# Kernel tuning notes

Hardware: AMD Instinct MI355X
Metric: run time of the kernel (lower is better)

The kernel has to match this reference:

```python
import jax, jax.numpy as jnp
import numpy as np

CUTOFF = 5.0
P_ENV = 5.0  # envelope exponent


def _build_triplets(src, dst, num_nodes):
    # Faithful numpy port of DimeNet.triplets (row=src=j, col=dst=i).
    # For each edge e=(j->i), enumerate in-edges f=(k->j) of node j, drop k==i.
    E = src.shape[0]
    order = np.argsort(dst, kind='stable')          # edge ids grouped by target node
    indeg = np.bincount(dst, minlength=num_nodes)
    ptr = np.concatenate([np.zeros(1, np.int64), np.cumsum(indeg)])
    counts = indeg[src]                              # num_triplets per edge e
    total = int(counts.sum())
    idx_ji = np.repeat(np.arange(E), counts)
    grp_start = np.repeat(np.cumsum(counts) - counts, counts)
    pos_in = np.arange(total) - grp_start
    idx_kj = order[ptr[src][idx_ji] + pos_in]        # in-edge ids f of node j
    idx_k = src[idx_kj]
    idx_j = src[idx_ji]
    idx_i = dst[idx_ji]
    mask = idx_i != idx_k
    return idx_i[mask], idx_j[mask], idx_k[mask]


def setup_inputs() -> dict:
    rng = np.random.default_rng(0)
    N, E, IN, H, NR, OUT = 50000, 400000, 128, 128, 6, 64
    src = rng.integers(0, N, E)
    dst = rng.integers(0, N, E)
    dst = np.where(dst == src, (dst + 1) % N, dst)   # no self loops
    idx_i, idx_j, idx_k = _build_triplets(src, dst, N)

    def W(*shape):
        fan_in = shape[-1]
        return jnp.asarray((rng.standard_normal(shape) / np.sqrt(fan_in)).astype(np.float32))

    return {
        'x': jnp.asarray(rng.standard_normal((N, IN)).astype(np.float32)),
        'pos': jnp.asarray((rng.standard_normal((N, 3)) * 3.0).astype(np.float32)),
        'freq': jnp.asarray(np.pi * np.arange(1, NR + 1, dtype=np.float32)),
        'Wx': jnp.asarray(rng.uniform(-np.sqrt(3), np.sqrt(3), (H, IN)).astype(np.float32)),
        'Wr': W(H, NR), 'br': jnp.zeros((H,), jnp.float32),
        'Wl': W(H, 3 * H), 'bl': jnp.zeros((H,), jnp.float32),
        'Wrbf': W(H, NR),
        'Wls': W(3, H, H), 'bls': jnp.zeros((3, H), jnp.float32),
        'Wout': W(OUT, H),
        'edge_src': jnp.asarray(src.astype(np.int32)),
        'edge_dst': jnp.asarray(dst.astype(np.int32)),
        'idx_i': jnp.asarray(idx_i.astype(np.int32)),
        'idx_j': jnp.asarray(idx_j.astype(np.int32)),
        'idx_k': jnp.asarray(idx_k.astype(np.int32)),
    }


def reference(x, pos, freq, Wx, Wr, br, Wl, bl, Wrbf, Wls, bls, Wout,
              edge_src, edge_dst, idx_i, idx_j, idx_k):
    swish = lambda t: t * jax.nn.sigmoid(t)
    num_nodes = x.shape[0]

    # edge distances: j,i = edge_index; dist = |pos[i]-pos[j]|
    d = jnp.sqrt(jnp.sum((pos[edge_dst] - pos[edge_src]) ** 2, axis=-1))  # [E]

    # triplet angles (computed as in original forward; sbf is a no-op)
    pi_ = pos[idx_i]
    v_ji = pos[idx_j] - pi_
    v_ki = pos[idx_k] - pi_
    a = jnp.sum(v_ji * v_ki, axis=-1)
    b = jnp.linalg.norm(jnp.cross(v_ji, v_ki), axis=-1)
    angle = jnp.arctan2(b, a)  # [T]

    # Bessel basis with polynomial envelope
    dn = (d / CUTOFF)[:, None]  # [E,1]
    p = P_ENV
    A = -(p + 1.0) * (p + 2.0) / 2.0
    B = p * (p + 2.0)
    C = -p * (p + 1.0) / 2.0
    dp = dn ** p
    env = 1.0 / dn + A * dp + B * dp * dn + C * dp * dn * dn
    rbf = env * jnp.sin(freq * dn)  # [E, NR]

    # EmbeddingBlock
    h = x @ Wx.T                                  # [N,H]
    rbf_h = swish(rbf @ Wr.T + br)                # [E,H]
    e = swish(jnp.concatenate([h[edge_dst], h[edge_src], rbf_h], axis=-1) @ Wl.T + bl)  # [E,H]

    # OutputBlock 0
    t = (rbf @ Wrbf.T) * e                        # [E,H]
    node = jax.ops.segment_sum(t, edge_dst, num_segments=num_nodes)  # [N,H]
    for k in range(Wls.shape[0]):
        node = swish(node @ Wls[k].T + bls[k])
    P = node @ Wout.T                             # [N,OUT]
    return P, angle
```

## Files before the change

kernel.cpp:

```cpp
#include <hip/hip_runtime.h>
#include <hip/hip_bf16.h>
#include <math.h>

#define H   128
#define NR  6
#define NOUT 64

typedef __attribute__((ext_vector_type(8))) short short8;
typedef __attribute__((ext_vector_type(4))) float floatx4;

__device__ __forceinline__ float swishf(float z) {
  float t = __expf(-z);
  return z * __builtin_amdgcn_rcpf(1.0f + t);
}

__device__ __forceinline__ ushort f2bf(float x) {
  __hip_bfloat16 b = __float2bfloat16(x);
  return *reinterpret_cast<ushort*>(&b);
}

__device__ __forceinline__ ushort f2bf_rne(float x) {
  unsigned int u = __float_as_uint(x);
  u += 0x7FFFu + ((u >> 16) & 1u);
  return (ushort)(u >> 16);
}

__device__ __forceinline__ float bf2f(ushort u) {
  unsigned int v = ((unsigned int)u) << 16;
  return __uint_as_float(v);
}

__device__ __forceinline__ void async_copy16(const void* g, void* l) {
  __builtin_amdgcn_global_load_lds(
      (const __attribute__((address_space(1))) unsigned int*)g,
      (__attribute__((address_space(3))) unsigned int*)l, 16, 0, 0);
}

__global__ void k_init(float4* __restrict__ nodeA, int n4, int* __restrict__ cnt, int n,
                       const float* __restrict__ Wl, const float* __restrict__ Wx,
                       const float* __restrict__ Wls, const float* __restrict__ Wout,
                       ushort* __restrict__ Wlbf,
                       ushort* __restrict__ Wxhi, ushort* __restrict__ Wxlo,
                       ushort* __restrict__ Wlshi, ushort* __restrict__ Wlslo,
                       ushort* __restrict__ Wouthi, ushort* __restrict__ Woutlo) {
  int i = blockIdx.x * blockDim.x + threadIdx.x;
  if (i < n4) nodeA[i] = make_float4(0.f, 0.f, 0.f, 0.f);
  if (i < n) cnt[i] = 0;
  int idx = i;
  if (idx < 49152) {
    Wlbf[idx] = f2bf(Wl[idx]);
    return;
  }
  idx -= 49152;
  if (idx < 16384) {
    float x = Wx[idx];
    ushort h = f2bf(x);
    Wxhi[idx] = h; Wxlo[idx] = f2bf(x - bf2f(h));
    return;
  }
  idx -= 16384;
  if (idx < 49152) {
    float x = Wls[idx];
    ushort h = f2bf(x);
    Wlshi[idx] = h; Wlslo[idx] = f2bf(x - bf2f(h));
    return;
  }
  idx -= 49152;
  if (idx < 8192) {
    float x = Wout[idx];
    ushort h = f2bf(x);
    Wouthi[idx] = h; Woutlo[idx] = f2bf(x - bf2f(h));
  }
}

__global__ void k_hist(const int* __restrict__ dst, int* __restrict__ cnt, int E) {
  int i = blockIdx.x * blockDim.x + threadIdx.x;
  if (i < E) atomicAdd(&cnt[dst[i]], 1);
}

__global__ __launch_bounds__(1024) void k_scanA(const int* __restrict__ cnt,
                                                int* __restrict__ cur,
                                                int* __restrict__ bsum, int N) {
  __shared__ int wsum[16];
  const int tid = threadIdx.x;
  const int gid = blockIdx.x * 1024 + tid;
  const int lane = tid & 63, wv = tid >> 6;
  int v0 = (gid < N) ? cnt[gid] : 0;
  int v = v0;
#pragma unroll
  for (int off = 1; off < 64; off <<= 1) {
    int t = __shfl_up(v, off, 64);
    if (lane >= off) v += t;
  }
  if (lane == 63) wsum[wv] = v;
  __syncthreads();
  if (wv == 0 && lane < 16) {
    int t = wsum[lane];
#pragma unroll
    for (int off = 1; off < 16; off <<= 1) {
      int u2 = __shfl_up(t, off, 64);
      if (lane >= off) t += u2;
    }
    wsum[lane] = t;
  }
  __syncthreads();
  int excl = (wv > 0 ? wsum[wv - 1] : 0) + (v - v0);
  if (gid < N) cur[gid] = excl;
  if (tid == 0) bsum[blockIdx.x] = wsum[15];
}

__global__ __launch_bounds__(256) void k_scatter_feat_ang(
    const float* __restrict__ pos, const int* __restrict__ esrc,
    const int* __restrict__ edst, const float* __restrict__ freq,
    int* __restrict__ cur, const int* __restrict__ bsum, int nscan,
    float* __restrict__ epk,
    int E, int EB,
    const int* __restrict__ ii, const int* __restrict__ jj, const int* __restrict__ kk,
    float* __restrict__ ang, int T) {
  if (blockIdx.x < (unsigned)EB) {
    __shared__ int boffS[64];
    {
      const int lane = threadIdx.x & 63;
      if (threadIdx.x < 64) {
        int v = (lane < nscan) ? bsum[lane] : 0;
        int v0 = v;
#pragma unroll
        for (int off = 1; off < 64; off <<= 1) {
          int t = __shfl_up(v, off, 64);
          if (lane >= off) v += t;
        }
        boffS[lane] = v - v0;
      }
    }
    __syncthreads();
    int i = blockIdx.x * 256 + threadIdx.x;
    if (i >= E) return;
    const int s = esrc[i], d = edst[i];
    const int p = atomicAdd(&cur[d], 1) + boffS[d >> 10];
    float dx = pos[d * 3 + 0] - pos[s * 3 + 0];
    float dy = pos[d * 3 + 1] - pos[s * 3 + 1];
    float dz = pos[d * 3 + 2] - pos[s * 3 + 2];
    float dist = sqrtf(dx * dx + dy * dy + dz * dz);
    float dn = dist * 0.2f;
    float inv = __builtin_amdgcn_rcpf(dn);
    float dn2 = dn * dn;
    float dp = dn2 * dn2 * dn;
    float env = inv - 21.0f * dp + 35.0f * dp * dn - 15.0f * dp * dn2;
    float rb[NR];
#pragma unroll
    for (int r = 0; r < NR; ++r) rb[r] = env * __sinf(freq[r] * dn);
    float4 w0 = make_float4(rb[0], rb[1], rb[2], rb[3]);
    float4 w1 = make_float4(rb[4], rb[5], __int_as_float(s), __int_as_float(d));
    *(float4*)&epk[(size_t)p * 8] = w0;
    *(float4*)&epk[(size_t)p * 8 + 4] = w1;
  } else {
    int t = (blockIdx.x - EB) * 256 + threadIdx.x;
    if (t >= T) return;
    int i = ii[t], j = jj[t], k = kk[t];
    float pix = pos[i * 3], piy = pos[i * 3 + 1], piz = pos[i * 3 + 2];
    float vjx = pos[j * 3] - pix, vjy = pos[j * 3 + 1] - piy, vjz = pos[j * 3 + 2] - piz;
    float vkx = pos[k * 3] - pix, vky = pos[k * 3 + 1] - piy, vkz = pos[k * 3 + 2] - piz;
    float a = vjx * vkx + vjy * vky + vjz * vkz;
    float cx = vjy * vkz - vjz * vky;
    float cy = vjz * vkx - vjx * vkz;
    float cz = vjx * vky - vjy * vkx;
    float b = sqrtf(cx * cx + cy * cy + cz * cz);
    ang[t] = atan2f(b, a);
  }
}

__global__ __launch_bounds__(512, 4) void k_x_gemm(
    const float* __restrict__ A,
    const ushort* __restrict__ Bhi,
    const ushort* __restrict__ Blo,
    ushort* __restrict__ C,
    int M) {
  __shared__ alignas(16) ushort Ah[128 * 32];
  __shared__ alignas(16) ushort Al[128 * 32];
  __shared__ alignas(16) ushort Bh[128 * 32];
  __shared__ alignas(16) ushort Bl[128 * 32];

  const int tid = threadIdx.x;
  const int m0 = blockIdx.x * 128;
  const int w = tid >> 6, lane = tid & 63;
  const int l15 = lane & 15, quad = lane >> 4;
  const int wm = (w >> 1) * 32;
  const int wn = (w & 1) * 64;

  floatx4 acc[2][4];
#pragma unroll
  for (int i = 0; i < 2; ++i)
#pragma unroll
    for (int j = 0; j < 4; ++j) acc[i][j] = floatx4{0.f, 0.f, 0.f, 0.f};

  for (int c = 0; c < 4; ++c) {
    const int kb = c * 32;
    {
      int row = tid >> 2, g = tid & 3;
      int m = m0 + row;
      float4 v0 = make_float4(0.f, 0.f, 0.f, 0.f), v1 = v0;
      if (m < M) {
        v0 = *(const float4*)&A[(size_t)m * 128 + kb + g * 8];
        v1 = *(const float4*)&A[(size_t)m * 128 + kb + g * 8 + 4];
      }
      float xs[8] = {v0.x, v0.y, v0.z, v0.w, v1.x, v1.y, v1.z, v1.w};
      short8 hi, lo;
#pragma unroll
      for (int j = 0; j < 8; ++j) {
        ushort h = f2bf_rne(xs[j]);
        hi[j] = (short)h;
        lo[j] = (short)f2bf_rne(xs[j] - bf2f(h));
      }
      int slot = row * 4 + (g ^ ((row >> 1) & 3));
      *(short8*)(Ah + slot * 8) = hi;
      *(short8*)(Al + slot * 8) = lo;
    }
    {
      int s = w * 64 + lane;
      int brow = s >> 2, gp = s & 3;
      int gg = gp ^ ((brow >> 1) & 3);
      int lb = __builtin_amdgcn_readfirstlane(w * 64);
      async_copy16((const void*)(Bhi + (size_t)brow * 128 + kb + gg * 8), (void*)(Bh + lb * 8));
      async_copy16((const void*)(Blo + (size_t)brow * 128 + kb + gg * 8), (void*)(Bl + lb * 8));
    }
    __syncthreads();
    short8 ah[2], al[2], bh[4], blv[4];
#pragma unroll
    for (int i = 0; i < 2; ++i) {
      int m = wm + i * 16 + l15;
      int slot = m * 4 + (quad ^ ((m >> 1) & 3));
      ah[i] = *(const short8*)(Ah + slot * 8);
      al[i] = *(const short8*)(Al + slot * 8);
    }
#pragma unroll
    for (int j = 0; j < 4; ++j) {
      int n = wn + j * 16 + l15;
      int slot = n * 4 + (quad ^ ((n >> 1) & 3));
      bh[j] = *(const short8*)(Bh + slot * 8);
      blv[j] = *(const short8*)(Bl + slot * 8);
    }
#pragma unroll
    for (int i = 0; i < 2; ++i)
#pragma unroll
      for (int j = 0; j < 4; ++j) {
        acc[i][j] = __builtin_amdgcn_mfma_f32_16x16x32_bf16(ah[i], bh[j], acc[i][j], 0, 0, 0);
        acc[i][j] = __builtin_amdgcn_mfma_f32_16x16x32_bf16(ah[i], blv[j], acc[i][j], 0, 0, 0);
        acc[i][j] = __builtin_amdgcn_mfma_f32_16x16x32_bf16(al[i], bh[j], acc[i][j], 0, 0, 0);
      }
    __syncthreads();
  }

#pragma unroll
  for (int i = 0; i < 2; ++i)
#pragma unroll
    for (int r = 0; r < 4; ++r) {
      int m = m0 + wm + i * 16 + quad * 4 + r;
      if (m < M) {
#pragma unroll
        for (int j = 0; j < 4; ++j) {
          int n = wn + j * 16 + l15;
          C[(size_t)m * 128 + n] = f2bf_rne(acc[i][j][r]);
        }
      }
    }
}

__global__ __launch_bounds__(512, 4) void k_node_mlp(
    const float* __restrict__ nodeA,
    const ushort* __restrict__ Wlshi,
    const ushort* __restrict__ Wlslo,
    const ushort* __restrict__ Wouthi,
    const ushort* __restrict__ Woutlo,
    const float* __restrict__ bls,
    float* __restrict__ P,
    int M) {
  __shared__ alignas(16) ushort AactH[64 * 16 * 8];
  __shared__ alignas(16) ushort AactL[64 * 16 * 8];
  __shared__ alignas(16) ushort Bh[128 * 4 * 8];
  __shared__ alignas(16) ushort Bl[128 * 4 * 8];
  __shared__ float blsS[3 * 128];

  const int tid = threadIdx.x;
  const int m0 = blockIdx.x * 64;
  const int w = tid >> 6, lane = tid & 63;
  const int l15 = lane & 15, quad = lane >> 4;
  const int wm = (w >> 2) * 32;
  const int wn = (w & 3) * 32;

  for (int i = tid; i < 3 * 128; i += 512) blsS[i] = bls[i];

  floatx4 acc[2][2];

  for (int p = 0; p < 3; ++p) {
    const ushort* Bhg = Wlshi + p * 128 * 128;
    const ushort* Blg = Wlslo + p * 128 * 128;
#pragma unroll
    for (int i = 0; i < 2; ++i)
#pragma unroll
      for (int j = 0; j < 2; ++j) acc[i][j] = floatx4{0.f, 0.f, 0.f, 0.f};

    for (int c = 0; c < 4; ++c) {
      const int kb = c * 32;
      {
        int s = w * 64 + lane;
        int brow = s >> 2, gp = s & 3;
        int gg = gp ^ ((brow >> 1) & 3);
        int lb = __builtin_amdgcn_readfirstlane(w * 64);
        async_copy16((const void*)(Bhg + (size_t)brow * 128 + kb + gg * 8), (void*)(Bh + lb * 8));
        async_copy16((const void*)(Blg + (size_t)brow * 128 + kb + gg * 8), (void*)(Bl + lb * 8));
      }
      __syncthreads();
      short8 ah[2], al[2];
      if (p == 0) {
#pragma unroll
        for (int i = 0; i < 2; ++i) {
          int m = m0 + wm + i * 16 + l15;
          float4 v0 = make_float4(0.f, 0.f, 0.f, 0.f), v1 = v0;
          if (m < M) {
            v0 = *(const float4*)&nodeA[(size_t)m * 128 + kb + quad * 8];
            v1 = *(const float4*)&nodeA[(size_t)m * 128 + kb + quad * 8 + 4];
          }
          float xs[8] = {v0.x, v0.y, v0.z, v0.w, v1.x, v1.y, v1.z, v1.w};
#pragma unroll
          for (int j = 0; j < 8; ++j) {
            ushort hh = f2bf_rne(xs[j]);
            ah[i][j] = (short)hh;
            al[i][j] = (short)f2bf_rne(xs[j] - bf2f(hh));
          }
        }
      } else {
#pragma unroll
        for (int i = 0; i < 2; ++i) {
          int arow = wm + i * 16 + l15;
          int g16 = c * 4 + quad;
          int slot = arow * 16 + (g16 ^ (arow & 15));
          ah[i] = *(const short8*)(AactH + slot * 8);
          al[i] = *(const short8*)(AactL + slot * 8);
        }
      }
      short8 bh[2], blv[2];
#pragma unroll
      for (int j = 0; j < 2; ++j) {
        int n = wn + j * 16 + l15;
        int slot = n * 4 + (quad ^ ((n >> 1) & 3));
        bh[j] = *(const short8*)(Bh + slot * 8);
        blv[j] = *(const short8*)(Bl + slot * 8);
      }
#pragma unroll
      for (int i = 0; i < 2; ++i)
#pragma unroll
        for (int j = 0; j < 2; ++j) {
          acc[i][j] = __builtin_amdgcn_mfma_f32_16x16x32_bf16(ah[i], bh[j], acc[i][j], 0, 0, 0);
          acc[i][j] = __builtin_amdgcn_mfma_f32_16x16x32_bf16(ah[i], blv[j], acc[i][j], 0, 0, 0);
          acc[i][j] = __builtin_amdgcn_mfma_f32_16x16x32_bf16(al[i], bh[j], acc[i][j], 0, 0, 0);
        }
      __syncthreads();
    }
#pragma unroll
    for (int i = 0; i < 2; ++i)
#pragma unroll
      for (int r = 0; r < 4; ++r) {
        int row = wm + i * 16 + quad * 4 + r;
#pragma unroll
        for (int j = 0; j < 2; ++j) {
          int col = wn + j * 16 + l15;
          float z = acc[i][j][r] + blsS[p * 128 + col];
          z = swishf(z);
          ushort hh = f2bf_rne(z);
          int slot = row * 16 + ((col >> 3) ^ (row & 15));
          AactH[slot * 8 + (col & 7)] = hh;
          AactL[slot * 8 + (col & 7)] = f2bf_rne(z - bf2f(hh));
        }
      }
    __syncthreads();
  }

  const int wn3 = (w & 3) * 16;
#pragma unroll
  for (int i = 0; i < 2; ++i) acc[i][0] = floatx4{0.f, 0.f, 0.f, 0.f};

  for (int c = 0; c < 4; ++c) {
    const int kb = c * 32;
    if (w < 4) {
      int s = w * 64 + lane;
      int brow = s >> 2, gp = s & 3;
      int gg = gp ^ ((brow >> 1) & 3);
      int lb = __builtin_amdgcn_readfirstlane(w * 64);
      async_copy16((const void*)(Wouthi + (size_t)brow * 128 + kb + gg * 8), (void*)(Bh + lb * 8));
      async_copy16((const void*)(Woutlo + (size_t)brow * 128 + kb + gg * 8), (void*)(Bl + lb * 8));
    }
    __syncthreads();
    short8 ah[2], al[2], bh, blv;
#pragma unroll
    for (int i = 0; i < 2; ++i) {
      int arow = wm + i * 16 + l15;
      int g16 = c * 4 + quad;
      int slot = arow * 16 + (g16 ^ (arow & 15));
      ah[i] = *(const short8*)(AactH + slot * 8);
      al[i] = *(const short8*)(AactL + slot * 8);
    }
    {
      int n = wn3 + l15;
      int slot = n * 4 + (quad ^ ((n >> 1) & 3));
      bh = *(const short8*)(Bh + slot * 8);
      blv = *(const short8*)(Bl + slot * 8);
    }
#pragma unroll
    for (int i = 0; i < 2; ++i) {
      acc[i][0] = __builtin_amdgcn_mfma_f32_16x16x32_bf16(ah[i], bh, acc[i][0], 0, 0, 0);
      acc[i][0] = __builtin_amdgcn_mfma_f32_16x16x32_bf16(ah[i], blv, acc[i][0], 0, 0, 0);
      acc[i][0] = __builtin_amdgcn_mfma_f32_16x16x32_bf16(al[i], bh, acc[i][0], 0, 0, 0);
    }
    __syncthreads();
  }
#pragma unroll
  for (int i = 0; i < 2; ++i)
#pragma unroll
    for (int r = 0; r < 4; ++r) {
      int m = m0 + wm + i * 16 + quad * 4 + r;
      if (m < M) {
        int n = wn3 + l15;
        P[(size_t)m * NOUT + n] = acc[i][0][r];
      }
    }
}

__global__ __launch_bounds__(512, 4) void k_edge_mfma(
    const ushort* __restrict__ hbf,
    const ushort* __restrict__ Wlbf,
    const float* __restrict__ bl,
    const float* __restrict__ epk,
    const float* __restrict__ Wr,
    const float* __restrict__ br,
    const float* __restrict__ Wrbf,
    float* __restrict__ node,
    int E, int nb, int perXcd) {
  __shared__ alignas(16) ushort ABs[33280];
  __shared__ float rbfS[128][6];
  __shared__ int dstS[128];
  __shared__ int srcS[128];

  const int bp = blockIdx.x;
  const int lb = (bp & 7) * perXcd + (bp >> 3);
  if (lb >= nb) return;

  ushort* As = ABs;
  ushort* Bs = ABs + 128 * 16 * 8;

  const int tid = threadIdx.x;
  const int e0 = lb * 128;

  if (tid < 128) {
    int e = min(e0 + tid, E - 1);
    const float* rec = epk + (size_t)e * 8;
    float4 r0 = *(const float4*)rec;
    float4 r1 = *(const float4*)(rec + 4);
    bool ok = (e0 + tid < E);
    rbfS[tid][0] = ok ? r0.x : 0.f;
    rbfS[tid][1] = ok ? r0.y : 0.f;
    rbfS[tid][2] = ok ? r0.z : 0.f;
    rbfS[tid][3] = ok ? r0.w : 0.f;
    rbfS[tid][4] = ok ? r1.x : 0.f;
    rbfS[tid][5] = ok ? r1.y : 0.f;
    srcS[tid] = __float_as_int(r1.z);
    dstS[tid] = __float_as_int(r1.w);
  }
  __syncthreads();

  const int w = tid >> 6;
  const int lane = tid & 63;
  const int l15 = lane & 15, quad = lane >> 4;
  const int wm = (w >> 1) * 32;
  const int wn = (w & 1) * 64;

  floatx4 acc[2][4];
#pragma unroll
  for (int i = 0; i < 2; ++i)
#pragma unroll
    for (int j = 0; j < 4; ++j) acc[i][j] = floatx4{0.f, 0.f, 0.f, 0.f};

  for (int c = 0; c < 3; ++c) {
#pragma unroll
    for (int i = 0; i < 4; ++i) {
      int u = w * 256 + i * 64 + lane;
      int nrow = u >> 4, gp = u & 15;
      int g = gp ^ (nrow & 15);
      const ushort* gsrc = Wlbf + (size_t)nrow * 384 + c * 128 + g * 8;
      int lbo = __builtin_amdgcn_readfirstlane(w * 256 + i * 64);
      async_copy16((const void*)gsrc, (void*)(Bs + lbo * 8));
    }
    if (c < 2) {
      const int* rowS = (c == 0) ? dstS : srcS;
#pragma unroll
      for (int i = 0; i < 4; ++i) {
        int u = w * 256 + i * 64 + lane;
        int nrow = u >> 4;
        int g = (u & 15) ^ (nrow & 15);
        int row = rowS[nrow];
        const ushort* gsrc = hbf + (size_t)row * H + g * 8;
        int lbo = __builtin_amdgcn_readfirstlane(w * 256 + i * 64);
        async_copy16((const void*)gsrc, (void*)(As + lbo * 8));
      }
    } else {
      const int colL = tid & 127;
      float w0 = Wr[colL * NR + 0], w1 = Wr[colL * NR + 1], w2 = Wr[colL * NR + 2];
      float w3 = Wr[colL * NR + 3], w4 = Wr[colL * NR + 4], w5 = Wr[colL * NR + 5];
      float bv = br[colL];
      const int r0 = (tid >> 7) * 32;
#pragma unroll
      for (int r = 0; r < 32; ++r) {
        int m = r0 + r;
        const float2* rp = (const float2*)&rbfS[m][0];
        float2 q0 = rp[0], q1 = rp[1], q2 = rp[2];
        float z = bv + q0.x * w0 + q0.y * w1 + q1.x * w2 + q1.y * w3 + q2.x * w4 + q2.y * w5;
        ushort hv = f2bf_rne(swishf(z));
        As[(m * 16 + ((colL >> 3) ^ (m & 15))) * 8 + (colL & 7)] = hv;
      }
    }
    __syncthreads();
#pragma unroll
    for (int s = 0; s < 4; ++s) {
      const int gg = s * 4 + quad;
      short8 af[2], bfr[4];
#pragma unroll
      for (int i = 0; i < 2; ++i) {
        int m = wm + i * 16 + l15;
        af[i] = *(const short8*)(As + (m * 16 + (gg ^ (m & 15))) * 8);
      }
#pragma unroll
      for (int j = 0; j < 4; ++j) {
        int n = wn + j * 16 + l15;
        bfr[j] = *(const short8*)(Bs + (n * 16 + (gg ^ (n & 15))) * 8);
      }
#pragma unroll
      for (int i = 0; i < 2; ++i)
#pragma unroll
        for (int j = 0; j < 4; ++j)
          acc[i][j] = __builtin_amdgcn_mfma_f32_16x16x32_bf16(af[i], bfr[j], acc[i][j], 0, 0, 0);
    }
    __syncthreads();
  }

  float* redS = (float*)ABs;
  float wt[4][NR], blv[4];
#pragma unroll
  for (int j = 0; j < 4; ++j) {
    int n = wn + j * 16 + l15;
    blv[j] = bl[n];
#pragma unroll
    for (int r = 0; r < NR; ++r) wt[j][r] = Wrbf[n * NR + r];
  }

#pragma unroll
  for (int i = 0; i < 2; ++i)
#pragma unroll
    for (int r = 0; r < 4; ++r) {
      int mg = wm + i * 16 + quad * 4 + r;
      float rb[NR];
#pragma unroll
      for (int q = 0; q < NR; ++q) rb[q] = rbfS[mg][q];
#pragma unroll
      for (int j = 0; j < 4; ++j) {
        float z = acc[i][j][r] + blv[j];
        float ev = swishf(z);
        float wv = 0.f;
#pragma unroll
        for (int q = 0; q < NR; ++q) wv += rb[q] * wt[j][q];
        redS[mg * 130 + wn + j * 16 + l15] = ev * wv;
      }
    }
  __syncthreads();

  {
    int cc = tid & 127, chunk = tid >> 7;
    int ml0 = chunk * 32;
    float s = 0.f;
    int prev = dstS[ml0];
#pragma unroll
    for (int ml = ml0; ml < ml0 + 32; ++ml) {
      int d = dstS[ml];
      float v = redS[ml * 130 + cc];
      if (d != prev) {
        atomicAdd(&node[(size_t)prev * H + cc], s);
        s = 0.f;
        prev = d;
      }
      s += v;
    }
    atomicAdd(&node[(size_t)prev * H + cc], s);
  }
}

extern "C" void kernel_launch(void* const* d_in, const int* in_sizes, int n_in,
                              void* d_out, int out_size, void* d_ws, size_t ws_size,
                              hipStream_t stream) {
  const float* x    = (const float*)d_in[0];
  const float* pos  = (const float*)d_in[1];
  const float* freq = (const float*)d_in[2];
  const float* Wx   = (const float*)d_in[3];
  const float* Wr   = (const float*)d_in[4];
  const float* br   = (const float*)d_in[5];
  const float* Wl   = (const float*)d_in[6];
  const float* bl   = (const float*)d_in[7];
  const float* Wrbf = (const float*)d_in[8];
  const float* Wls  = (const float*)d_in[9];
  const float* bls  = (const float*)d_in[10];
  const float* Wout = (const float*)d_in[11];
  const int* esrc = (const int*)d_in[12];
  const int* edst = (const int*)d_in[13];
  const int* ii   = (const int*)d_in[14];
  const int* jjv  = (const int*)d_in[15];
  const int* kkv  = (const int*)d_in[16];

  const int N = in_sizes[0] / H;
  const int E = in_sizes[12];
  const int T = in_sizes[14];

  float* out   = (float*)d_out;
  float* P     = out;
  float* angle = out + (size_t)N * NOUT;

  float* ws = (float*)d_ws;
  float* epk   = ws; ws += (size_t)E * 8;
  float* nodeA = ws; ws += (size_t)N * H;
  ushort* u = (ushort*)ws;
  ushort* hbf    = u; u += (size_t)N * H;
  ushort* Wlbf   = u; u += 3 * H * H;
  ushort* Wxhi   = u; u += H * H;
  ushort* Wxlo   = u; u += H * H;
  ushort* Wlshi  = u; u += 3 * H * H;
  ushort* Wlslo  = u; u += 3 * H * H;
  ushort* Wouthi = u; u += NOUT * H;
  ushort* Woutlo = u; u += NOUT * H;
  int* ip = (int*)u;
  int* cnt   = ip; ip += N;
  int* cur   = ip; ip += N;
  int* bsum  = ip; ip += 256;

  {
    int n4 = N * H / 4;
    k_init<<<(n4 + 255) / 256, 256, 0, stream>>>((float4*)nodeA, n4, cnt, N,
                                                 Wl, Wx, Wls, Wout, Wlbf,
                                                 Wxhi, Wxlo, Wlshi, Wlslo, Wouthi, Woutlo);
  }

  const int nscan = (N + 1023) / 1024;
  k_hist<<<(E + 255) / 256, 256, 0, stream>>>(edst, cnt, E);
  k_scanA<<<nscan, 1024, 0, stream>>>(cnt, cur, bsum, N);

  {
    int EB = (E + 255) / 256;
    int TB = (T + 255) / 256;
    k_scatter_feat_ang<<<EB + TB, 256, 0, stream>>>(pos, esrc, edst, freq, cur,
                                                    bsum, nscan, epk, E, EB,
                                                    ii, jjv, kkv, angle, T);
  }

  k_x_gemm<<<(N + 127) / 128, 512, 0, stream>>>(x, Wxhi, Wxlo, hbf, N);

  {
    int nb = (E + 127) / 128;
    int perXcd = (nb + 7) / 8;
    int grid = perXcd * 8;
    k_edge_mfma<<<grid, 512, 0, stream>>>(hbf, Wlbf, bl, epk, Wr, br, Wrbf,
                                          nodeA, E, nb, perXcd);
  }

  k_node_mlp<<<(N + 63) / 64, 512, 0, stream>>>(nodeA, Wlshi, Wlslo, Wouthi, Woutlo,
                                                bls, P, N);
}
```

Measured before the change: 341.4 us.

## Precompute per-node projections of h to shrink edge GEMM K dimension

New measurement: 349.3 us. 1.02x slower.

```diff
diff --git a/kernel.cpp b/kernel.cpp
--- a/kernel.cpp
+++ b/kernel.cpp
@@ -265,6 +265,77 @@
     }
 }
 
+__global__ __launch_bounds__(512, 4) void k_z_gemm(
+    const ushort* __restrict__ hbf,
+    const ushort* __restrict__ Wlbf,
+    int koff,
+    ushort* __restrict__ Z,
+    int M) {
+  __shared__ alignas(16) ushort Asm[128 * 32];
+  __shared__ alignas(16) ushort Bsm[128 * 32];
+
+  const int tid = threadIdx.x;
+  const int m0 = blockIdx.x * 128;
+  const int w = tid >> 6, lane = tid & 63;
+  const int l15 = lane & 15, quad = lane >> 4;
+  const int wm = (w >> 1) * 32;
+  const int wn = (w & 1) * 64;
+
+  floatx4 acc[2][4];
+#pragma unroll
+  for (int i = 0; i < 2; ++i)
+#pragma unroll
+    for (int j = 0; j < 4; ++j) acc[i][j] = floatx4{0.f, 0.f, 0.f, 0.f};
+
+  for (int c = 0; c < 4; ++c) {
+    const int kb = c * 32;
+    {
+      int s = w * 64 + lane;
+      int brow = s >> 2, gp = s & 3;
+      int gg = gp ^ ((brow >> 1) & 3);
+      int lb = __builtin_amdgcn_readfirstlane(w * 64);
+      async_copy16((const void*)(hbf + (size_t)(m0 + brow) * 128 + kb + gg * 8),
+                   (void*)(Asm + lb * 8));
+      async_copy16((const void*)(Wlbf + (size_t)brow * 384 + koff + kb + gg * 8),
+                   (void*)(Bsm + lb * 8));
+    }
+    __syncthreads();
+    short8 af[2], bf[4];
+#pragma unroll
+    for (int i = 0; i < 2; ++i) {
+      int m = wm + i * 16 + l15;
+      int slot = m * 4 + (quad ^ ((m >> 1) & 3));
+      af[i] = *(const short8*)(Asm + slot * 8);
+    }
+#pragma unroll
+    for (int j = 0; j < 4; ++j) {
+      int n = wn + j * 16 + l15;
+      int slot = n * 4 + (quad ^ ((n >> 1) & 3));
+      bf[j] = *(const short8*)(Bsm + slot * 8);
+    }
+#pragma unroll
+    for (int i = 0; i < 2; ++i)
+#pragma unroll
+      for (int j = 0; j < 4; ++j)
+        acc[i][j] = __builtin_amdgcn_mfma_f32_16x16x32_bf16(af[i], bf[j], acc[i][j], 0, 0, 0);
+    __syncthreads();
+  }
+
+#pragma unroll
+  for (int i = 0; i < 2; ++i)
+#pragma unroll
+    for (int r = 0; r < 4; ++r) {
+      int m = m0 + wm + i * 16 + quad * 4 + r;
+      if (m < M) {
+#pragma unroll
+        for (int j = 0; j < 4; ++j) {
+          int n = wn + j * 16 + l15;
+          Z[(size_t)m * 128 + n] = f2bf_rne(acc[i][j][r]);
+        }
+      }
+    }
+}
+
 __global__ __launch_bounds__(512, 4) void k_node_mlp(
     const float* __restrict__ nodeA,
     const ushort* __restrict__ Wlshi,
@@ -426,7 +497,8 @@
 }
 
 __global__ __launch_bounds__(512, 4) void k_edge_mfma(
-    const ushort* __restrict__ hbf,
+    const ushort* __restrict__ Zdb,
+    const ushort* __restrict__ Zsb,
     const ushort* __restrict__ Wlbf,
     const float* __restrict__ bl,
     const float* __restrict__ epk,
@@ -473,73 +545,79 @@
   const int wm = (w >> 1) * 32;
   const int wn = (w & 1) * 64;
 
+#pragma unroll
+  for (int i = 0; i < 4; ++i) {
+    int u = w * 256 + i * 64 + lane;
+    int nrow = u >> 4;
+    int g = (u & 15) ^ (nrow & 15);
+    int lbo = __builtin_amdgcn_readfirstlane(w * 256 + i * 64);
+    async_copy16((const void*)(Zdb + (size_t)dstS[nrow] * H + g * 8), (void*)(As + lbo * 8));
+    async_copy16((const void*)(Zsb + (size_t)srcS[nrow] * H + g * 8), (void*)(Bs + lbo * 8));
+  }
+  __syncthreads();
+
   floatx4 acc[2][4];
 #pragma unroll
   for (int i = 0; i < 2; ++i)
 #pragma unroll
-    for (int j = 0; j < 4; ++j) acc[i][j] = floatx4{0.f, 0.f, 0.f, 0.f};
-
-  for (int c = 0; c < 3; ++c) {
-#pragma unroll
-    for (int i = 0; i < 4; ++i) {
-      int u = w * 256 + i * 64 + lane;
-      int nrow = u >> 4, gp = u & 15;
-      int g = gp ^ (nrow & 15);
-      const ushort* gsrc = Wlbf + (size_t)nrow * 384 + c * 128 + g * 8;
-      int lbo = __builtin_amdgcn_readfirstlane(w * 256 + i * 64);
-      async_copy16((const void*)gsrc, (void*)(Bs + lbo * 8));
-    }
-    if (c < 2) {
-      const int* rowS = (c == 0) ? dstS : srcS;
-#pragma unroll
-      for (int i = 0; i < 4; ++i) {
-        int u = w * 256 + i * 64 + lane;
-        int nrow = u >> 4;
-        int g = (u & 15) ^ (nrow & 15);
-        int row = rowS[nrow];
-        const ushort* gsrc = hbf + (size_t)row * H + g * 8;
-        int lbo = __builtin_amdgcn_readfirstlane(w * 256 + i * 64);
-        async_copy16((const void*)gsrc, (void*)(As + lbo * 8));
-      }
-    } else {
-      const int colL = tid & 127;
-      float w0 = Wr[colL * NR + 0], w1 = Wr[colL * NR + 1], w2 = Wr[colL * NR + 2];
-      float w3 = Wr[colL * NR + 3], w4 = Wr[colL * NR + 4], w5 = Wr[colL * NR + 5];
-      float bv = br[colL];
-      const int r0 = (tid >> 7) * 32;
-#pragma unroll
-      for (int r = 0; r < 32; ++r) {
-        int m = r0 + r;
-        const float2* rp = (const float2*)&rbfS[m][0];
-        float2 q0 = rp[0], q1 = rp[1], q2 = rp[2];
-        float z = bv + q0.x * w0 + q0.y * w1 + q1.x * w2 + q1.y * w3 + q2.x * w4 + q2.y * w5;
-        ushort hv = f2bf_rne(swishf(z));
-        As[(m * 16 + ((colL >> 3) ^ (m & 15))) * 8 + (colL & 7)] = hv;
-      }
-    }
-    __syncthreads();
-#pragma unroll
-    for (int s = 0; s < 4; ++s) {
-      const int gg = s * 4 + quad;
-      short8 af[2], bfr[4];
-#pragma unroll
-      for (int i = 0; i < 2; ++i) {
-        int m = wm + i * 16 + l15;
-        af[i] = *(const short8*)(As + (m * 16 + (gg ^ (m & 15))) * 8);
-      }
+    for (int r = 0; r < 4; ++r) {
+      int mg = wm + i * 16 + quad * 4 + r;
 #pragma unroll
       for (int j = 0; j < 4; ++j) {
-        int n = wn + j * 16 + l15;
-        bfr[j] = *(const short8*)(Bs + (n * 16 + (gg ^ (n & 15))) * 8);
-      }
-#pragma unroll
-      for (int i = 0; i < 2; ++i)
-#pragma unroll
-        for (int j = 0; j < 4; ++j)
-          acc[i][j] = __builtin_amdgcn_mfma_f32_16x16x32_bf16(af[i], bfr[j], acc[i][j], 0, 0, 0);
-    }
-    __syncthreads();
-  }
+        int col = wn + j * 16 + l15;
+        int sa = (mg * 16 + ((col >> 3) ^ (mg & 15))) * 8 + (col & 7);
+        acc[i][j][r] = bf2f(As[sa]) + bf2f(Bs[sa]);
+      }
+    }
+  __syncthreads();
+
+#pragma unroll
+  for (int i = 0; i < 4; ++i) {
+    int u = w * 256 + i * 64 + lane;
+    int nrow = u >> 4, gp = u & 15;
+    int g = gp ^ (nrow & 15);
+    const ushort* gsrc = Wlbf + (size_t)nrow * 384 + 256 + g * 8;
+    int lbo = __builtin_amdgcn_readfirstlane(w * 256 + i * 64);
+    async_copy16((const void*)gsrc, (void*)(Bs + lbo * 8));
+  }
+  {
+    const int colL = tid & 127;
+    float w0 = Wr[colL * NR + 0], w1 = Wr[colL * NR + 1], w2 = Wr[colL * NR + 2];
+    float w3 = Wr[colL * NR + 3], w4 = Wr[colL * NR + 4], w5 = Wr[colL * NR + 5];
+    float bv = br[colL];
+    const int r0 = (tid >> 7) * 32;
+#pragma unroll
+    for (int r = 0; r < 32; ++r) {
+      int m = r0 + r;
+      const float2* rp = (const float2*)&rbfS[m][0];
+      float2 q0 = rp[0], q1 = rp[1], q2 = rp[2];
+      float z = bv + q0.x * w0 + q0.y * w1 + q1.x * w2 + q1.y * w3 + q2.x * w4 + q2.y * w5;
+      ushort hv = f2bf_rne(swishf(z));
+      As[(m * 16 + ((colL >> 3) ^ (m & 15))) * 8 + (colL & 7)] = hv;
+    }
+  }
+  __syncthreads();
+#pragma unroll
+  for (int s = 0; s < 4; ++s) {
+    const int gg = s * 4 + quad;
+    short8 af[2], bfr[4];
+#pragma unroll
+    for (int i = 0; i < 2; ++i) {
+      int m = wm + i * 16 + l15;
+      af[i] = *(const short8*)(As + (m * 16 + (gg ^ (m & 15))) * 8);
+    }
+#pragma unroll
+    for (int j = 0; j < 4; ++j) {
+      int n = wn + j * 16 + l15;
+      bfr[j] = *(const short8*)(Bs + (n * 16 + (gg ^ (n & 15))) * 8);
+    }
+#pragma unroll
+    for (int i = 0; i < 2; ++i)
+#pragma unroll
+      for (int j = 0; j < 4; ++j)
+        acc[i][j] = __builtin_amdgcn_mfma_f32_16x16x32_bf16(af[i], bfr[j], acc[i][j], 0, 0, 0);
+  }
+  __syncthreads();
 
   float* redS = (float*)ABs;
   float wt[4][NR], blv[4];
@@ -625,6 +703,8 @@
   float* nodeA = ws; ws += (size_t)N * H;
   ushort* u = (ushort*)ws;
   ushort* hbf    = u; u += (size_t)N * H;
+  ushort* Zdb    = u; u += (size_t)N * H;
+  ushort* Zsb    = u; u += (size_t)N * H;
   ushort* Wlbf   = u; u += 3 * H * H;
   ushort* Wxhi   = u; u += H * H;
   ushort* Wxlo   = u; u += H * H;
@@ -658,11 +738,14 @@
 
   k_x_gemm<<<(N + 127) / 128, 512, 0, stream>>>(x, Wxhi, Wxlo, hbf, N);
 
+  k_z_gemm<<<(N + 127) / 128, 512, 0, stream>>>(hbf, Wlbf, 0, Zdb, N);
+  k_z_gemm<<<(N + 127) / 128, 512, 0, stream>>>(hbf, Wlbf, 128, Zsb, N);
+
   {
     int nb = (E + 127) / 128;
     int perXcd = (nb + 7) / 8;
     int grid = perXcd * 8;
-    k_edge_mfma<<<grid, 512, 0, stream>>>(hbf, Wlbf, bl, epk, Wr, br, Wrbf,
+    k_edge_mfma<<<grid, 512, 0, stream>>>(Zdb, Zsb, Wlbf, bl, epk, Wr, br, Wrbf,
                                           nodeA, E, nb, perXcd);
   }
 
```
